# Performance work log

Measured on AMD Instinct MI355X. Metric: run time of the kernel, lower is better.

The kernel has to match this reference:

```python
import jax, jax.numpy as jnp
import numpy as np

B, L, D = 16, 1024, 768
MAX_MENTION_LEN = 10
NEG_INF = -jnp.inf


def _static_bounds_and_keep(L, max_len):
    # mention_bounds[s, e] = (s, e); keep pairs with e - s + 1 <= max_len
    s = np.arange(L)[:, None]
    e = np.arange(L)[None, :]
    keep = ((e - s + 1) <= max_len).reshape(-1)  # static bool (L*L,)
    bounds = np.stack([np.broadcast_to(s, (L, L)), np.broadcast_to(e, (L, L))], axis=-1).reshape(-1, 2)
    return bounds[keep], keep


def setup_inputs() -> dict:
    key = jax.random.key(0)
    k1, k2, k3 = jax.random.split(key, 3)
    bert_output = jax.random.normal(k1, (B, L, D), dtype=jnp.float32)
    # contiguous prefix mask (padded-batch style), lengths in [L//2, L]
    lengths = jax.random.randint(k2, (B,), L // 2, L + 1)
    input_mask = jnp.arange(L)[None, :] < lengths[:, None]  # (B, L) bool
    W = jax.random.normal(k3, (3, D), dtype=jnp.float32) * 0.02  # Linear(768, 3) weight
    b = jnp.zeros((3,), dtype=jnp.float32)
    return {"bert_output": bert_output, "input_mask": input_mask, "W": W, "b": b}


def reference(bert_output, input_mask, W, b):
    Bc, Lc, _ = bert_output.shape
    logits = jnp.einsum('bld,kd->blk', bert_output, W) + b  # (B, L, 3)
    start_lp = jnp.where(input_mask, logits[..., 0], NEG_INF)
    end_lp = jnp.where(input_mask, logits[..., 1], NEG_INF)
    mention_lp = jnp.where(input_mask, logits[..., 2], NEG_INF)

    # inclusive cumsum at end index e; exclusive cumsum at start index s
    incl = jnp.cumsum(mention_lp, axis=1)  # (B, L)
    excl = jnp.concatenate([jnp.zeros((Bc, 1), incl.dtype), incl[:, :-1]], axis=1)  # (B, L)

    # scores[b, s, e] = start[s] + end[e] + sum_{i=s..e} mention[i]
    scores = start_lp[:, :, None] + end_lp[:, None, :] + incl[:, None, :] - excl[:, :, None]

    s_idx = jnp.arange(Lc)[:, None]
    e_idx = jnp.arange(Lc)[None, :]
    sizes = e_idx - s_idx + 1  # (L, L)
    valid = (sizes > 0)[None, :, :] & input_mask[:, None, :]  # (B, L, L)
    scores = jnp.where(valid, scores, NEG_INF)  # also overwrites any NaN from inf arithmetic, as torch does

    scores = scores.reshape(Bc, Lc * Lc)
    bounds_np, keep = _static_bounds_and_keep(Lc, MAX_MENTION_LEN)  # static numpy
    scores = scores[:, keep]  # (B, K) with static K
    bounds = jnp.broadcast_to(jnp.asarray(bounds_np, dtype=jnp.int64)[None], (Bc, bounds_np.shape[0], 2))
    return scores, bounds
```

## Files before the change

kernel.cpp:

```cpp
#include <hip/hip_runtime.h>
#include <math.h>

#define B_      16
#define L_      1024
#define D_      768
#define MAXLEN  10
#define NKEEP     533971
#define S_BREAK   1014
#define OFF_BREAK 523731

#define NEG_SENTINEL (-1.0e30f)

__device__ __forceinline__ int row_off(int s) {
    return (s < S_BREAK) ? ((s * (s + 19)) >> 1)
                         : OFF_BREAK + (s - S_BREAK) * L_;
}

__global__ __launch_bounds__(256) void k_logits(
    const float* __restrict__ X, const float* __restrict__ W,
    const float* __restrict__ bias,
    float* __restrict__ sArr, float* __restrict__ eArr, float* __restrict__ mArr)
{
    const int wave = threadIdx.x >> 6;
    const int lane = threadIdx.x & 63;
    const int row  = blockIdx.x * 4 + wave;
    const float4* x4 = (const float4*)(X + (size_t)row * D_);
    const float4* w0 = (const float4*)(W);
    const float4* w1 = (const float4*)(W + D_);
    const float4* w2 = (const float4*)(W + 2 * D_);
    float a0 = 0.f, a1 = 0.f, a2 = 0.f;
#pragma unroll
    for (int k = 0; k < 3; ++k) {
        const int f = lane + 64 * k;
        const float4 x = x4[f];
        float4 u = w0[f]; a0 += x.x*u.x + x.y*u.y + x.z*u.z + x.w*u.w;
        float4 v = w1[f]; a1 += x.x*v.x + x.y*v.y + x.z*v.z + x.w*v.w;
        float4 t = w2[f]; a2 += x.x*t.x + x.y*t.y + x.z*t.z + x.w*t.w;
    }
#pragma unroll
    for (int off = 32; off; off >>= 1) {
        a0 += __shfl_xor(a0, off, 64);
        a1 += __shfl_xor(a1, off, 64);
        a2 += __shfl_xor(a2, off, 64);
    }
    if (lane == 0) {
        sArr[row] = a0 + bias[0];
        eArr[row] = a1 + bias[1];
        mArr[row] = a2 + bias[2];
    }
}

__global__ __launch_bounds__(1024) void k_scan(float* __restrict__ mArr)
{
    __shared__ float buf[L_];
    const int b = blockIdx.x, t = threadIdx.x;
    buf[t] = mArr[b * L_ + t];
    __syncthreads();
    for (int off = 1; off < L_; off <<= 1) {
        const float v = (t >= off) ? buf[t - off] : 0.0f;
        __syncthreads();
        buf[t] += v;
        __syncthreads();
    }
    mArr[b * L_ + t] = buf[t];
}

__global__ __launch_bounds__(256) void k_scores(
    const float* __restrict__ sArr, const float* __restrict__ eArr,
    const float* __restrict__ incl, const int* __restrict__ mask,
    float* __restrict__ outScores, float2* __restrict__ outBounds)
{
    const int s = blockIdx.x;
    const int b = blockIdx.y;
    const int cs  = min(s + MAXLEN, L_);
    const int off = row_off(s);
    const float slog = sArr[b * L_ + s];
    const float excl = (s > 0) ? incl[b * L_ + s - 1] : 0.0f;
    float*  dstS = outScores + (size_t)b * NKEEP + off;
    float2* dstB = outBounds + (size_t)b * NKEEP + off;
    const float sf = (float)s;
    for (int e = threadIdx.x; e < cs; e += 256) {
        const bool valid = (e >= s) && (mask[b * L_ + e] != 0);
        const float v = ((slog + eArr[b * L_ + e]) + incl[b * L_ + e]) - excl;
        dstS[e] = valid ? v : NEG_SENTINEL;
        dstB[e] = make_float2(sf, (float)e);
    }
}

extern "C" void kernel_launch(void* const* d_in, const int* in_sizes, int n_in,
                              void* d_out, int out_size, void* d_ws, size_t ws_size,
                              hipStream_t stream)
{
    const float* X    = (const float*)d_in[0];
    const int*   mask = (const int*)d_in[1];
    const float* W    = (const float*)d_in[2];
    const float* bias = (const float*)d_in[3];

    float* sArr = (float*)d_ws;
    float* eArr = sArr + B_ * L_;
    float* mArr = eArr + B_ * L_;

    float*  outScores = (float*)d_out;
    float2* outBounds = (float2*)((char*)d_out +
                                  (size_t)B_ * NKEEP * sizeof(float));

    hipLaunchKernelGGL(k_logits, dim3(B_ * L_ / 4), dim3(256), 0, stream,
                       X, W, bias, sArr, eArr, mArr);
    hipLaunchKernelGGL(k_scan, dim3(B_), dim3(1024), 0, stream, mArr);
    hipLaunchKernelGGL(k_scores, dim3(L_, B_), dim3(256), 0, stream,
                       sArr, eArr, mArr, mask, outScores, outBounds);
}
```

Measured before the change: 160.6 us.

## Flatten pair kernel over kept indices and use single-wave scan

The scores kernel now gives each thread one kept (s,e) index, recovering s and e from the flat index with a sqrt-based inverse. It then loops over all batches, writing scores and bounds with nontemporal stores, so every wave is fully used instead of most threads idling on short rows. The scan becomes one 64-lane wave per batch, doing a serial 16-element prefix per lane plus a shuffle scan, which removes repeated block barriers. The cost is per-thread index decoding and strided per-batch stores.

```diff
diff --git a/kernel.cpp b/kernel.cpp
--- a/kernel.cpp
+++ b/kernel.cpp
@@ -10,6 +10,8 @@
 #define OFF_BREAK 523731
 
 #define NEG_SENTINEL (-1.0e30f)
+
+typedef float f32x2 __attribute__((ext_vector_type(2)));
 
 __device__ __forceinline__ int row_off(int s) {
     return (s < S_BREAK) ? ((s * (s + 19)) >> 1)
@@ -50,40 +52,63 @@
     }
 }
 
-__global__ __launch_bounds__(1024) void k_scan(float* __restrict__ mArr)
+__global__ __launch_bounds__(64) void k_scan(float* __restrict__ mArr)
 {
-    __shared__ float buf[L_];
-    const int b = blockIdx.x, t = threadIdx.x;
-    buf[t] = mArr[b * L_ + t];
-    __syncthreads();
-    for (int off = 1; off < L_; off <<= 1) {
-        const float v = (t >= off) ? buf[t - off] : 0.0f;
-        __syncthreads();
-        buf[t] += v;
-        __syncthreads();
+    const int b = blockIdx.x, lane = threadIdx.x;
+    float4* p = (float4*)(mArr + b * L_ + lane * 16);
+    float x[16];
+#pragma unroll
+    for (int i = 0; i < 4; ++i) {
+        const float4 v = p[i];
+        x[4*i+0] = v.x; x[4*i+1] = v.y; x[4*i+2] = v.z; x[4*i+3] = v.w;
     }
-    mArr[b * L_ + t] = buf[t];
+#pragma unroll
+    for (int i = 1; i < 16; ++i) x[i] += x[i-1];
+    const float tot = x[15];
+    float inc = tot;
+#pragma unroll
+    for (int off = 1; off < 64; off <<= 1) {
+        const float t = __shfl_up(inc, off, 64);
+        if (lane >= off) inc += t;
+    }
+    const float prefix = inc - tot;
+#pragma unroll
+    for (int i = 0; i < 4; ++i) {
+        p[i] = make_float4(x[4*i+0] + prefix, x[4*i+1] + prefix,
+                           x[4*i+2] + prefix, x[4*i+3] + prefix);
+    }
 }
 
-__global__ __launch_bounds__(256) void k_scores(
+__global__ __launch_bounds__(256) void k_pairs(
     const float* __restrict__ sArr, const float* __restrict__ eArr,
     const float* __restrict__ incl, const int* __restrict__ mask,
-    float* __restrict__ outScores, float2* __restrict__ outBounds)
+    float* __restrict__ outScores, f32x2* __restrict__ outBounds)
 {
-    const int s = blockIdx.x;
-    const int b = blockIdx.y;
-    const int cs  = min(s + MAXLEN, L_);
-    const int off = row_off(s);
-    const float slog = sArr[b * L_ + s];
-    const float excl = (s > 0) ? incl[b * L_ + s - 1] : 0.0f;
-    float*  dstS = outScores + (size_t)b * NKEEP + off;
-    float2* dstB = outBounds + (size_t)b * NKEEP + off;
-    const float sf = (float)s;
-    for (int e = threadIdx.x; e < cs; e += 256) {
-        const bool valid = (e >= s) && (mask[b * L_ + e] != 0);
+    const int idx = blockIdx.x * 256 + threadIdx.x;
+    if (idx >= NKEEP) return;
+    int s, e;
+    if (idx >= OFF_BREAK) {
+        const int r = idx - OFF_BREAK;
+        s = S_BREAK + (r >> 10);
+        e = r & (L_ - 1);
+    } else {
+        const float f = sqrtf((float)(8 * idx + 361));
+        s = (int)((f - 19.0f) * 0.5f);
+        while (row_off(s + 1) <= idx) ++s;
+        while (row_off(s) > idx) --s;
+        e = idx - row_off(s);
+    }
+    f32x2 bnd; bnd.x = (float)s; bnd.y = (float)e;
+    const bool ege = (e >= s);
+#pragma unroll
+    for (int b = 0; b < B_; ++b) {
+        const bool valid = ege && (mask[b * L_ + e] != 0);
+        const float slog = sArr[b * L_ + s];
+        const float excl = (s > 0) ? incl[b * L_ + s - 1] : 0.0f;
         const float v = ((slog + eArr[b * L_ + e]) + incl[b * L_ + e]) - excl;
-        dstS[e] = valid ? v : NEG_SENTINEL;
-        dstB[e] = make_float2(sf, (float)e);
+        const size_t o = (size_t)b * NKEEP + idx;
+        __builtin_nontemporal_store(valid ? v : NEG_SENTINEL, &outScores[o]);
+        __builtin_nontemporal_store(bnd, &outBounds[o]);
     }
 }
 
@@ -100,13 +125,13 @@
     float* eArr = sArr + B_ * L_;
     float* mArr = eArr + B_ * L_;
 
-    float*  outScores = (float*)d_out;
-    float2* outBounds = (float2*)((char*)d_out +
-                                  (size_t)B_ * NKEEP * sizeof(float));
+    float* outScores = (float*)d_out;
+    f32x2* outBounds = (f32x2*)((char*)d_out +
+                                (size_t)B_ * NKEEP * sizeof(float));
 
     hipLaunchKernelGGL(k_logits, dim3(B_ * L_ / 4), dim3(256), 0, stream,
                        X, W, bias, sArr, eArr, mArr);
-    hipLaunchKernelGGL(k_scan, dim3(B_), dim3(1024), 0, stream, mArr);
-    hipLaunchKernelGGL(k_scores, dim3(L_, B_), dim3(256), 0, stream,
+    hipLaunchKernelGGL(k_scan, dim3(B_), dim3(64), 0, stream, mArr);
+    hipLaunchKernelGGL(k_pairs, dim3((NKEEP + 255) / 256), dim3(256), 0, stream,
                        sArr, eArr, mArr, mask, outScores, outBounds);
 }
```

New measurement: 168.0 us. +4.6%, slower.
